# Optimization experiments

Measured on AMD Instinct MI355X. Metric: run time of the kernel, lower is better.

Reference implementation:

```python
import jax, jax.numpy as jnp
import numpy as np

DIM = 768
NUM_HEADS = 12
HEAD_DIM = DIM // NUM_HEADS
SCALE = HEAD_DIM ** -0.5
B, N = 8, 1024


def setup_inputs() -> dict:
    key = jax.random.key(0)
    k1, k2, k3, k4 = jax.random.split(key, 4)
    s = 1.0 / np.sqrt(DIM)
    return {
        "x": jax.random.normal(k1, (B, N, DIM), dtype=jnp.float32),
        "w_qkv": jax.random.normal(k2, (DIM, 3 * DIM), dtype=jnp.float32) * s,  # qkv_bias=False
        "w_proj": jax.random.normal(k3, (DIM, DIM), dtype=jnp.float32) * s,
        "b_proj": jax.random.normal(k4, (DIM,), dtype=jnp.float32) * 0.01,
    }


def reference(x, w_qkv, w_proj, b_proj):
    Bb, Nn, C = x.shape
    qkv = x @ w_qkv  # [B, N, 3C]
    qkv = qkv.reshape(Bb, Nn, 3, NUM_HEADS, HEAD_DIM)
    q = qkv[:, :, 0].transpose(0, 2, 1, 3)  # [B, H, N, d]
    k = qkv[:, :, 1].transpose(0, 2, 1, 3)
    v = qkv[:, :, 2].transpose(0, 2, 1, 3)
    attn = jnp.einsum("bhqd,bhkd->bhqk", q, k) * SCALE
    attn = jax.nn.softmax(attn, axis=-1)  # dropout p=0 -> identity
    out = jnp.einsum("bhqk,bhkd->bhqd", attn, v)
    out = out.transpose(0, 2, 1, 3).reshape(Bb, Nn, C)
    return out @ w_proj + b_proj
```

## Files before the change

kernel.cpp:

```cpp
#include <hip/hip_runtime.h>
#include <stdint.h>

typedef __attribute__((ext_vector_type(8))) __bf16 bf16x8;
typedef __attribute__((ext_vector_type(8))) unsigned short u16x8;
typedef __attribute__((ext_vector_type(4))) unsigned short u16x4;
typedef __attribute__((ext_vector_type(4))) short s16x4;
typedef __attribute__((ext_vector_type(4))) float f32x4;

typedef unsigned int u32_as1 __attribute__((address_space(1)));
typedef unsigned int u32_as3 __attribute__((address_space(3)));

__device__ __forceinline__ unsigned short f2bf(float f) {
  unsigned int u = __float_as_uint(f);
  u += 0x7fffu + ((u >> 16) & 1u);
  return (unsigned short)(u >> 16);
}

__device__ __forceinline__ bf16x8 ld_frag(const unsigned short* p) {
  return __builtin_bit_cast(bf16x8, *(const u16x8*)p);
}

__device__ __forceinline__ f32x4 mfma16(s16x4 a, s16x4 b, f32x4 c) {
#if __has_builtin(__builtin_amdgcn_mfma_f32_16x16x16bf16_1k)
  return __builtin_amdgcn_mfma_f32_16x16x16bf16_1k(a, b, c, 0, 0, 0);
#elif __has_builtin(__builtin_amdgcn_mfma_f32_16x16x16_bf16_1k)
  return __builtin_amdgcn_mfma_f32_16x16x16_bf16_1k(a, b, c, 0, 0, 0);
#else
  asm volatile("v_mfma_f32_16x16x16_bf16 %0, %1, %2, %0"
               : "+v"(c) : "v"(a), "v"(b));
  return c;
#endif
}

__device__ __forceinline__ float fast_exp2(float x) {
#if __has_builtin(__builtin_amdgcn_exp2f)
  return __builtin_amdgcn_exp2f(x);
#else
  return exp2f(x);
#endif
}

__device__ __forceinline__ void async16(const void* g, void* l) {
  const u32_as1* gp = (const u32_as1*)(uintptr_t)g;
  u32_as3* lp = (u32_as3*)(uintptr_t)l;
  __builtin_amdgcn_global_load_lds(gp, lp, 16, 0, 0);
}

__device__ __forceinline__ void lds_barrier() {
  asm volatile("s_waitcnt lgkmcnt(0)\ns_barrier" ::: "memory");
}
template <int N> __device__ __forceinline__ void wait_vmcnt() {
  if constexpr (N == 0) asm volatile("s_waitcnt vmcnt(0)" ::: "memory");
  else if constexpr (N == 4) asm volatile("s_waitcnt vmcnt(4)" ::: "memory");
}

__global__ __launch_bounds__(256) void prep_kernel(
    const float* __restrict__ x, const float* __restrict__ w_qkv,
    const float* __restrict__ w_proj, u16x4* __restrict__ x_bf,
    unsigned short* __restrict__ wqkvT, unsigned short* __restrict__ wprojT) {
  const int bid = blockIdx.x;
  const int t = threadIdx.x;
  if (bid < 6144) {
    const int i = bid * 256 + t;
    float4 v = ((const float4*)x)[i];
    u16x4 o;
    o[0] = f2bf(v.x); o[1] = f2bf(v.y); o[2] = f2bf(v.z); o[3] = f2bf(v.w);
    x_bf[i] = o;
    return;
  }
  __shared__ float tile[32][33];
  const float* w; unsigned short* wt; int N, bx, by;
  if (bid < 6144 + 1728) { const int r = bid - 6144; w = w_qkv; wt = wqkvT; N = 2304; bx = r % 72; by = r / 72; }
  else                   { const int r = bid - 7872; w = w_proj; wt = wprojT; N = 768; bx = r % 24; by = r / 24; }
  const int n0 = bx * 32, k0 = by * 32;
  const int tx = t & 31, ty = t >> 5;
#pragma unroll
  for (int r = 0; r < 4; r++)
    tile[ty + r * 8][tx] = w[(k0 + ty + r * 8) * N + n0 + tx];
  __syncthreads();
#pragma unroll
  for (int r = 0; r < 4; r++)
    wt[(n0 + ty + r * 8) * 768 + k0 + tx] = f2bf(tile[tx][ty + r * 8]);
}

template <int EPI, int NT, int NBLK, int MINW>
__global__ __launch_bounds__(256, MINW) void gemm_bt(
    const unsigned short* __restrict__ A, const unsigned short* __restrict__ Bt,
    unsigned short* __restrict__ qb, unsigned short* __restrict__ kb,
    unsigned short* __restrict__ vtb, float* __restrict__ outp,
    const float* __restrict__ bias) {
  constexpr int STAGE = 4096 + NT * 2048;
  constexpr int NK = 24;
  constexpr int NLD = 2 + NT;
  __shared__ unsigned short smem[2 * STAGE];

  const int t = threadIdx.x;
  const int lane = t & 63, w = t >> 6;
  const int quad = lane >> 4, l15 = lane & 15;

  const int bid = blockIdx.x;
  const int xcd = bid & 7, slot = bid >> 3;
  const int m0 = (xcd * 8 + slot / NBLK) * 128;
  const int n0 = (slot % NBLK) * (NT * 64);
  const int wm = (w & 1) * 64, wn = (w >> 1) * (NT * 32);

  f32x4 acc[4][NT * 2];
  const f32x4 fzero = {0.f, 0.f, 0.f, 0.f};
#pragma unroll
  for (int i = 0; i < 4; i++)
#pragma unroll
    for (int j = 0; j < NT * 2; j++) acc[i][j] = fzero;

  const int srow = w * 16 + (lane >> 2);
  const int scol = (((lane & 3) - (srow >> 1)) & 3) * 8;
  const unsigned short* Ag = A + (m0 + srow) * 768 + scol;
  const unsigned short* Bg = Bt + (n0 + srow) * 768 + scol;
  const int ldso = w * 512 + lane * 8;

  u16x8 rb[2][NLD];

  auto g2r = [&](int k, u16x8* r) {
    r[0] = *(const u16x8*)(Ag + k * 32);
    r[1] = *(const u16x8*)(Ag + 64 * 768 + k * 32);
#pragma unroll
    for (int f = 0; f < NT; f++)
      r[2 + f] = *(const u16x8*)(Bg + f * 64 * 768 + k * 32);
  };
  auto r2l = [&](int k, const u16x8* r) {
    unsigned short* As = smem + (k & 1) * STAGE;
    *(u16x8*)(As + ldso) = r[0];
    *(u16x8*)(As + ldso + 2048) = r[1];
#pragma unroll
    for (int f = 0; f < NT; f++)
      *(u16x8*)(As + 4096 + ldso + f * 2048) = r[2 + f];
  };

  g2r(0, rb[0]);
  g2r(1, rb[1]);
  r2l(0, rb[0]);
  lds_barrier();
  g2r(2, rb[0]);

#pragma unroll
  for (int k = 0; k < NK; ++k) {
    const unsigned short* As = smem + (k & 1) * STAGE;
    const unsigned short* Bs = As + 4096;

    bf16x8 af[4], bfr[NT * 2];
#pragma unroll
    for (int i = 0; i < 4; i++) {
      const int row = wm + i * 16 + l15;
      af[i] = ld_frag(As + row * 32 + (((quad + (row >> 1)) & 3) << 3));
    }
#pragma unroll
    for (int j = 0; j < NT * 2; j++) {
      const int row = wn + j * 16 + l15;
      bfr[j] = ld_frag(Bs + row * 32 + (((quad + (row >> 1)) & 3) << 3));
    }
#pragma unroll
    for (int i = 0; i < 4; i++)
#pragma unroll
      for (int j = 0; j < NT * 2; j++)
        acc[i][j] = __builtin_amdgcn_mfma_f32_16x16x32_bf16(af[i], bfr[j], acc[i][j], 0, 0, 0);

    if (k + 1 < NK) r2l(k + 1, rb[(k + 1) & 1]);
    if (k + 3 < NK) g2r(k + 3, rb[(k + 1) & 1]);
    if (k + 1 < NK) lds_barrier();
  }

#pragma unroll
  for (int i = 0; i < 4; i++) {
    const int gmb = m0 + wm + i * 16 + quad * 4;
#pragma unroll
    for (int j = 0; j < NT * 2; j++) {
      const int gc = n0 + wn + j * 16 + l15;
#pragma unroll
      for (int r = 0; r < 4; r++) {
        const int gm = gmb + r;
        float v = acc[i][j][r];
        if (EPI == 0) {
          const int b = gm >> 10, tok = gm & 1023;
          const int which = (gc >= 1536) ? 2 : (gc >= 768 ? 1 : 0);
          const int rem = gc - which * 768;
          const int h = rem >> 6, d = rem & 63;
          const int bh = b * 12 + h;
          const unsigned short bv = f2bf(v);
          if (which == 0)      qb[(bh << 16) + (tok << 6) + d] = bv;
          else if (which == 1) kb[(bh << 16) + (tok << 6) + d] = bv;
          else                 vtb[(bh << 16) + (d << 10) + tok] = bv;
        } else {
          outp[gm * 768 + gc] = v + bias[gc];
        }
      }
    }
  }
}

#define SWZC(row, c) (((row) << 6) + ((((c) + (row)) & 7) << 3))
#define C2 0.1803368801111244f

__global__ __launch_bounds__(256, 3) void attn_kernel(
    const unsigned short* __restrict__ qb, const unsigned short* __restrict__ kb,
    const unsigned short* __restrict__ vtb, unsigned short* __restrict__ aout) {
  __shared__ unsigned short smem[3 * 8192];

  const int t = threadIdx.x;
  const int lane = t & 63, w = t >> 6;
  const int quad = lane >> 4, l15 = lane & 15;
  const int bh = blockIdx.x;
  const int b = bh / 12, h = bh - b * 12;
  const int q0 = blockIdx.y * 128;
  const int base = bh << 16;

  bf16x8 qf[2][2];
#pragma unroll
  for (int qt = 0; qt < 2; qt++)
#pragma unroll
    for (int s = 0; s < 2; s++)
      qf[qt][s] = ld_frag(qb + base + ((q0 + w * 32 + qt * 16 + l15) << 6) +
                          s * 32 + quad * 8);

  f32x4 oacc[4][2];
  const f32x4 fzero = {0.f, 0.f, 0.f, 0.f};
#pragma unroll
  for (int dt = 0; dt < 4; dt++) { oacc[dt][0] = fzero; oacc[dt][1] = fzero; }
  float lsum0 = 0.f, lsum1 = 0.f;

  const int srow = t >> 3, schk = t & 7;
  const int c0 = ((schk - srow) & 7) * 8;
  const int c1 = ((schk - (srow + 32)) & 7) * 8;

  auto fillkv = [&](int tile, int buf) {
    const int kv0 = tile * 64;
    unsigned short* Ks = smem + buf * 8192;
    unsigned short* Vts = Ks + 4096;
    async16(kb + base + ((kv0 + srow) << 6) + c0, Ks + t * 8);
    async16(kb + base + ((kv0 + srow + 32) << 6) + c1, Ks + 2048 + t * 8);
    async16(vtb + base + (srow << 10) + kv0 + c0, Vts + t * 8);
    async16(vtb + base + ((srow + 32) << 10) + kv0 + c1, Vts + 2048 + t * 8);
  };

  fillkv(0, 0);
  fillkv(1, 1);
  int cur = 0;
  for (int it = 0; it < 16; ++it) {
    if (it < 15) wait_vmcnt<4>(); else wait_vmcnt<0>();
    asm volatile("s_barrier" ::: "memory");
    if (it + 2 < 16) {
      int tgt = cur + 2; if (tgt >= 3) tgt -= 3;
      fillkv(it + 2, tgt);
    }
    const unsigned short* Ks = smem + cur * 8192;
    const unsigned short* Vts = Ks + 4096;

    f32x4 st[4][2];
#pragma unroll
    for (int tc = 0; tc < 4; tc++) { st[tc][0] = fzero; st[tc][1] = fzero; }
#pragma unroll
    for (int s = 0; s < 2; s++) {
#pragma unroll
      for (int tc = 0; tc < 4; tc++) {
        const bf16x8 kf = ld_frag(Ks + SWZC(tc * 16 + l15, s * 4 + quad));
        st[tc][0] = __builtin_amdgcn_mfma_f32_16x16x32_bf16(kf, qf[0][s], st[tc][0], 0, 0, 0);
        st[tc][1] = __builtin_amdgcn_mfma_f32_16x16x32_bf16(kf, qf[1][s], st[tc][1], 0, 0, 0);
      }
    }

    s16x4 pf[4][2];
#pragma unroll
    for (int tc = 0; tc < 4; tc++) {
#pragma unroll
      for (int qt = 0; qt < 2; qt++) {
        const float p0 = fast_exp2(st[tc][qt][0] * C2);
        const float p1 = fast_exp2(st[tc][qt][1] * C2);
        const float p2 = fast_exp2(st[tc][qt][2] * C2);
        const float p3 = fast_exp2(st[tc][qt][3] * C2);
        const float ps = (p0 + p1) + (p2 + p3);
        if (qt == 0) lsum0 += ps; else lsum1 += ps;
        s16x4 pk;
        pk[0] = (short)f2bf(p0); pk[1] = (short)f2bf(p1);
        pk[2] = (short)f2bf(p2); pk[3] = (short)f2bf(p3);
        pf[tc][qt] = pk;
      }
    }

#pragma unroll
    for (int tc = 0; tc < 4; tc++) {
#pragma unroll
      for (int dt = 0; dt < 4; dt++) {
        const int row = dt * 16 + l15;
        const int addr = (row << 6) + ((((tc * 2 + (quad >> 1)) + row) & 7) << 3) +
                         ((quad & 1) << 2);
        const s16x4 vf = *(const s16x4*)(Vts + addr);
        oacc[dt][0] = mfma16(vf, pf[tc][0], oacc[dt][0]);
        oacc[dt][1] = mfma16(vf, pf[tc][1], oacc[dt][1]);
      }
    }

    cur += 1; if (cur == 3) cur = 0;
  }

  lsum0 += __shfl_xor(lsum0, 16); lsum0 += __shfl_xor(lsum0, 32);
  lsum1 += __shfl_xor(lsum1, 16); lsum1 += __shfl_xor(lsum1, 32);
  const float inv0 = 1.f / lsum0, inv1 = 1.f / lsum1;

  __syncthreads();
  unsigned short* Ot = smem;
#pragma unroll
  for (int dt = 0; dt < 4; dt++) {
#pragma unroll
    for (int qt = 0; qt < 2; qt++) {
      const float inv = qt == 0 ? inv0 : inv1;
      const int qrow = (w * 32 + qt * 16 + l15) * 72 + dt * 16 + quad * 4;
#pragma unroll
      for (int r = 0; r < 4; r++)
        Ot[qrow + r] = f2bf(oacc[dt][qt][r] * inv);
    }
  }
  __syncthreads();
#pragma unroll
  for (int it = 0; it < 4; it++) {
    const int q = it * 32 + (t >> 3);
    const int d0 = (t & 7) * 8;
    const u16x8 v = *(const u16x8*)(Ot + q * 72 + d0);
    *(u16x8*)(aout + (b * 1024 + q0 + q) * 768 + h * 64 + d0) = v;
  }
}

extern "C" void kernel_launch(void* const* d_in, const int* in_sizes, int n_in,
                              void* d_out, int out_size, void* d_ws, size_t ws_size,
                              hipStream_t stream) {
  (void)in_sizes; (void)n_in; (void)out_size; (void)ws_size;
  const float* x = (const float*)d_in[0];
  const float* w_qkv = (const float*)d_in[1];
  const float* w_proj = (const float*)d_in[2];
  const float* b_proj = (const float*)d_in[3];
  float* out = (float*)d_out;

  char* ws = (char*)d_ws;
  unsigned short* x_bf   = (unsigned short*)(ws);
  unsigned short* wqkvT  = (unsigned short*)(ws + 12582912);
  unsigned short* wprojT = (unsigned short*)(ws + 16121856);
  unsigned short* qb     = (unsigned short*)(ws + 17301504);
  unsigned short* kb     = (unsigned short*)(ws + 29884416);
  unsigned short* vtb    = (unsigned short*)(ws + 42467328);
  unsigned short* aout   = x_bf;

  prep_kernel<<<8448, 256, 0, stream>>>(x, w_qkv, w_proj, (u16x4*)x_bf, wqkvT, wprojT);
  gemm_bt<0, 2, 18, 3><<<1152, 256, 0, stream>>>(x_bf, wqkvT, qb, kb, vtb, nullptr, nullptr);
  attn_kernel<<<dim3(96, 8), 256, 0, stream>>>(qb, kb, vtb, aout);
  gemm_bt<1, 1, 12, 4><<<768, 256, 0, stream>>>(aout, wprojT, nullptr, nullptr, nullptr, out, b_proj);
}
```

Measured before the change: 194.1 us.

## Use direct global-to-LDS async loads with triple-buffered GEMM pipeline

```diff
diff --git a/kernel.cpp b/kernel.cpp
--- a/kernel.cpp
+++ b/kernel.cpp
@@ -46,12 +46,13 @@
   __builtin_amdgcn_global_load_lds(gp, lp, 16, 0, 0);
 }
 
-__device__ __forceinline__ void lds_barrier() {
-  asm volatile("s_waitcnt lgkmcnt(0)\ns_barrier" ::: "memory");
-}
 template <int N> __device__ __forceinline__ void wait_vmcnt() {
-  if constexpr (N == 0) asm volatile("s_waitcnt vmcnt(0)" ::: "memory");
+  if constexpr (N == 0)      asm volatile("s_waitcnt vmcnt(0)" ::: "memory");
+  else if constexpr (N == 2) asm volatile("s_waitcnt vmcnt(2)" ::: "memory");
+  else if constexpr (N == 3) asm volatile("s_waitcnt vmcnt(3)" ::: "memory");
   else if constexpr (N == 4) asm volatile("s_waitcnt vmcnt(4)" ::: "memory");
+  else if constexpr (N == 6) asm volatile("s_waitcnt vmcnt(6)" ::: "memory");
+  else if constexpr (N == 8) asm volatile("s_waitcnt vmcnt(8)" ::: "memory");
 }
 
 __global__ __launch_bounds__(256) void prep_kernel(
@@ -92,7 +93,7 @@
   constexpr int STAGE = 4096 + NT * 2048;
   constexpr int NK = 24;
   constexpr int NLD = 2 + NT;
-  __shared__ unsigned short smem[2 * STAGE];
+  __shared__ unsigned short smem[3 * STAGE];
 
   const int t = threadIdx.x;
   const int lane = t & 63, w = t >> 6;
@@ -117,33 +118,26 @@
   const unsigned short* Bg = Bt + (n0 + srow) * 768 + scol;
   const int ldso = w * 512 + lane * 8;
 
-  u16x8 rb[2][NLD];
-
-  auto g2r = [&](int k, u16x8* r) {
-    r[0] = *(const u16x8*)(Ag + k * 32);
-    r[1] = *(const u16x8*)(Ag + 64 * 768 + k * 32);
+  auto fill = [&](int k, int stg) {
+    unsigned short* As = smem + stg * STAGE;
+    async16(Ag + k * 32, As + ldso);
+    async16(Ag + 64 * 768 + k * 32, As + ldso + 2048);
 #pragma unroll
     for (int f = 0; f < NT; f++)
-      r[2 + f] = *(const u16x8*)(Bg + f * 64 * 768 + k * 32);
+      async16(Bg + f * 64 * 768 + k * 32, As + 4096 + ldso + f * 2048);
   };
-  auto r2l = [&](int k, const u16x8* r) {
-    unsigned short* As = smem + (k & 1) * STAGE;
-    *(u16x8*)(As + ldso) = r[0];
-    *(u16x8*)(As + ldso + 2048) = r[1];
-#pragma unroll
-    for (int f = 0; f < NT; f++)
-      *(u16x8*)(As + 4096 + ldso + f * 2048) = r[2 + f];
-  };
-
-  g2r(0, rb[0]);
-  g2r(1, rb[1]);
-  r2l(0, rb[0]);
-  lds_barrier();
-  g2r(2, rb[0]);
+
+  fill(0, 0);
+  fill(1, 1);
 
 #pragma unroll
   for (int k = 0; k < NK; ++k) {
-    const unsigned short* As = smem + (k & 1) * STAGE;
+    if (k + 1 < NK) wait_vmcnt<NLD>();
+    else            wait_vmcnt<0>();
+    asm volatile("s_barrier" ::: "memory");
+    if (k + 2 < NK) fill(k + 2, (k + 2) % 3);
+
+    const unsigned short* As = smem + (k % 3) * STAGE;
     const unsigned short* Bs = As + 4096;
 
     bf16x8 af[4], bfr[NT * 2];
@@ -162,10 +156,6 @@
 #pragma unroll
       for (int j = 0; j < NT * 2; j++)
         acc[i][j] = __builtin_amdgcn_mfma_f32_16x16x32_bf16(af[i], bfr[j], acc[i][j], 0, 0, 0);
-
-    if (k + 1 < NK) r2l(k + 1, rb[(k + 1) & 1]);
-    if (k + 3 < NK) g2r(k + 3, rb[(k + 1) & 1]);
-    if (k + 1 < NK) lds_barrier();
   }
 
 #pragma unroll
```

Result: no change. 194.5 us (+0.2%).
